# Performance work log

Measured on AMD Instinct MI355X. Metric: run time of the kernel, lower is better.

## Reference

```python
import jax, jax.numpy as jnp
import numpy as np
import math

B, L, IN_DIM = 2, 2048, 32
D_MODEL, NHEAD, D_FF, N_LAYERS, NUM_CLASSES = 256, 8, 1024, 2, 8
FACTOR = 5
D_K = D_MODEL // NHEAD
U = min(L, int(FACTOR * math.log(L)))  # ProbSparse top-k size = 38
LN_EPS = 1e-5


def setup_inputs() -> dict:
    key = jax.random.key(0)
    ks = jax.random.split(key, 16)
    s = 0.02
    d = {
        "x": jax.random.normal(ks[0], (B, L, IN_DIM), jnp.float32),
        "emb_w": jax.random.normal(ks[1], (IN_DIM, D_MODEL), jnp.float32) * s,
        "emb_b": jnp.zeros((D_MODEL,), jnp.float32),
        "wq": jax.random.normal(ks[2], (N_LAYERS, D_MODEL, D_MODEL), jnp.float32) * s,
        "bq": jnp.zeros((N_LAYERS, D_MODEL), jnp.float32),
        "wk": jax.random.normal(ks[3], (N_LAYERS, D_MODEL, D_MODEL), jnp.float32) * s,
        "bk": jnp.zeros((N_LAYERS, D_MODEL), jnp.float32),
        "wv": jax.random.normal(ks[4], (N_LAYERS, D_MODEL, D_MODEL), jnp.float32) * s,
        "bv": jnp.zeros((N_LAYERS, D_MODEL), jnp.float32),
        "wo": jax.random.normal(ks[5], (N_LAYERS, D_MODEL, D_MODEL), jnp.float32) * s,
        "bo": jnp.zeros((N_LAYERS, D_MODEL), jnp.float32),
        "ln1_g": jnp.ones((N_LAYERS, D_MODEL), jnp.float32),
        "ln1_b": jnp.zeros((N_LAYERS, D_MODEL), jnp.float32),
        "ln2_g": jnp.ones((N_LAYERS, D_MODEL), jnp.float32),
        "ln2_b": jnp.zeros((N_LAYERS, D_MODEL), jnp.float32),
        "ff1_w": jax.random.normal(ks[6], (N_LAYERS, D_MODEL, D_FF), jnp.float32) * s,
        "ff1_b": jnp.zeros((N_LAYERS, D_FF), jnp.float32),
        "ff2_w": jax.random.normal(ks[7], (N_LAYERS, D_FF, D_MODEL), jnp.float32) * s,
        "ff2_b": jnp.zeros((N_LAYERS, D_MODEL), jnp.float32),
        "dec_w": jax.random.normal(ks[8], (D_MODEL, NUM_CLASSES), jnp.float32) * s,
        "dec_b": jnp.zeros((NUM_CLASSES,), jnp.float32),
    }
    return d


def _pos_encoding(L, d):
    pos = jnp.arange(L, dtype=jnp.float32)[:, None]              # [L,1]
    div = jnp.exp(jnp.arange(0, d, 2, dtype=jnp.float32) * (-math.log(10000.0) / d))
    sin, cos = jnp.sin(pos * div), jnp.cos(pos * div)            # [L,d/2]
    return jnp.stack([sin, cos], axis=-1).reshape(L, d)          # interleave sin/cos


def _layernorm(h, g, b):
    m = jnp.mean(h, axis=-1, keepdims=True)
    v = jnp.mean((h - m) ** 2, axis=-1, keepdims=True)
    return (h - m) * jax.lax.rsqrt(v + LN_EPS) * g + b


def _prob_sparse_attn(h, wq, bq, wk, bk, wv, bv, wo, bo):
    Bb, Ll, _ = h.shape
    q = (h @ wq + bq).reshape(Bb, Ll, NHEAD, D_K).transpose(0, 2, 1, 3)  # [B,H,L,D]
    k = (h @ wk + bk).reshape(Bb, Ll, NHEAD, D_K).transpose(0, 2, 1, 3)
    v = (h @ wv + bv).reshape(Bb, Ll, NHEAD, D_K).transpose(0, 2, 1, 3)
    scores = jnp.einsum('bhld,bhmd->bhlm', q, k) / math.sqrt(D_K)        # [B,H,L,L]
    thr = jax.lax.top_k(scores, U)[0][..., -1:]                          # U-th largest per row
    scores = jnp.where(scores >= thr, scores, -jnp.inf)
    attn = jax.nn.softmax(scores, axis=-1)
    ctx = jnp.einsum('bhlm,bhmd->bhld', attn, v)
    ctx = ctx.transpose(0, 2, 1, 3).reshape(Bb, Ll, D_MODEL)
    return ctx @ wo + bo


def reference(x, emb_w, emb_b, wq, bq, wk, bk, wv, bv, wo, bo,
              ln1_g, ln1_b, ln2_g, ln2_b, ff1_w, ff1_b, ff2_w, ff2_b,
              dec_w, dec_b):
    h = (x @ emb_w + emb_b) * math.sqrt(D_MODEL)
    h = h + _pos_encoding(h.shape[1], D_MODEL)[None]
    for l in range(N_LAYERS):
        a = _prob_sparse_attn(h, wq[l], bq[l], wk[l], bk[l], wv[l], bv[l], wo[l], bo[l])
        h = _layernorm(h + a, ln1_g[l], ln1_b[l])
        ff = jax.nn.relu(h @ ff1_w[l] + ff1_b[l]) @ ff2_w[l] + ff2_b[l]
        h = _layernorm(h + ff, ln2_g[l], ln2_b[l])
    return h @ dec_w + dec_b
```

## Files before the change

kernel.cpp:

```cpp
#include <hip/hip_runtime.h>
#include <math.h>

#define D_MODEL 256
#define NHEAD   8
#define D_K     32
#define LSEQ    2048
#define BATCH   2
#define ROWS    (BATCH * LSEQ)
#define D_FF    1024
#define UTOP    38
#define CAP     128

__global__ __launch_bounds__(256) void k_embed(const float* __restrict__ x,
                                               const float* __restrict__ w,
                                               const float* __restrict__ b,
                                               float* __restrict__ h) {
    int row = blockIdx.x;
    int l   = row & (LSEQ - 1);
    int d   = threadIdx.x;
    __shared__ float xs[32];
    if (d < 32) xs[d] = x[row * 32 + d];
    __syncthreads();
    float acc = 0.f;
#pragma unroll
    for (int i = 0; i < 32; ++i) acc += xs[i] * w[i * D_MODEL + d];
    acc = (acc + b[d]) * 16.0f;
    int m = d >> 1;
    float div = expf(-(float)(2 * m) * (9.210340371976184f / 256.0f));
    float ang = (float)l * div;
    float pe = (d & 1) ? cosf(ang) : sinf(ang);
    h[row * D_MODEL + d] = acc + pe;
}

template <int MODE>
__device__ __forceinline__ void gemm_body(const float* __restrict__ A, int lda,
                                          const float* __restrict__ W, int N,
                                          const float* __restrict__ bias, bool doBias,
                                          float* __restrict__ C, int K,
                                          int m0, int n0) {
    __shared__ float As[16][68];
    __shared__ float Ws[16][68];
    const int t  = threadIdx.x;
    const int tx = t & 15, ty = t >> 4;
    float acc[4][4] = {};
    for (int k0 = 0; k0 < K; k0 += 16) {
        {
            int mr = t >> 2, kc = (t & 3) * 4;
            float4 av = *(const float4*)&A[(size_t)(m0 + mr) * lda + k0 + kc];
            As[kc + 0][mr] = av.x; As[kc + 1][mr] = av.y;
            As[kc + 2][mr] = av.z; As[kc + 3][mr] = av.w;
            int kr = t >> 4, nc = (t & 15) * 4;
            *(float4*)&Ws[kr][nc] = *(const float4*)&W[(size_t)(k0 + kr) * N + n0 + nc];
        }
        __syncthreads();
#pragma unroll
        for (int k = 0; k < 16; ++k) {
            float4 a4 = *(const float4*)&As[k][ty * 4];
            float4 w4 = *(const float4*)&Ws[k][tx * 4];
            float av[4] = {a4.x, a4.y, a4.z, a4.w};
            float wv[4] = {w4.x, w4.y, w4.z, w4.w};
#pragma unroll
            for (int i = 0; i < 4; ++i)
#pragma unroll
                for (int j = 0; j < 4; ++j) acc[i][j] += av[i] * wv[j];
        }
        __syncthreads();
    }
#pragma unroll
    for (int i = 0; i < 4; ++i) {
        int row = m0 + ty * 4 + i;
#pragma unroll
        for (int j = 0; j < 4; ++j) {
            int col = n0 + tx * 4 + j;
            float v = acc[i][j];
            if (doBias) v += bias[col];
            if (MODE == 1) v = fmaxf(v, 0.f);
            if (MODE == 2) {
                int bb = row >> 11, ll = row & (LSEQ - 1);
                int hh = col >> 5, dd = col & 31;
                C[(((size_t)(bb * NHEAD + hh) * LSEQ) + ll) * D_K + dd] = v;
            } else {
                C[(size_t)row * N + col] = v;
            }
        }
    }
}

__global__ __launch_bounds__(256) void k_qkv(const float* __restrict__ A,
                                             const float* __restrict__ wq,
                                             const float* __restrict__ wk,
                                             const float* __restrict__ wv,
                                             const float* __restrict__ bq,
                                             const float* __restrict__ bk,
                                             const float* __restrict__ bv,
                                             float* __restrict__ out) {
    int z = blockIdx.z;
    const float* W = z == 0 ? wq : (z == 1 ? wk : wv);
    const float* B = z == 0 ? bq : (z == 1 ? bk : bv);
    gemm_body<2>(A, 256, W, 256, B, true, out + (size_t)z * (1 << 20), 256,
                 blockIdx.x * 64, blockIdx.y * 64);
}

__global__ __launch_bounds__(256) void k_gemm_sk(const float* __restrict__ A, int lda,
                                                 const float* __restrict__ W,
                                                 const float* __restrict__ bias,
                                                 float* __restrict__ Cbase,
                                                 int N, int Ksub) {
    int z = blockIdx.z;
    gemm_body<0>(A + (size_t)z * Ksub, lda, W + (size_t)z * Ksub * N, N, bias, z == 0,
                 Cbase + (size_t)z * (1 << 20), Ksub, blockIdx.x * 64, blockIdx.y * 64);
}

__global__ __launch_bounds__(256) void k_ff1(const float* __restrict__ A,
                                             const float* __restrict__ W,
                                             const float* __restrict__ bias,
                                             float* __restrict__ C) {
    gemm_body<1>(A, 256, W, 1024, bias, true, C, 256, blockIdx.x * 64, blockIdx.y * 64);
}

__device__ __forceinline__ unsigned int sortkey(float f) {
    unsigned int u = __float_as_uint(f);
    return (u & 0x80000000u) ? ~u : (u | 0x80000000u);
}
__device__ __forceinline__ float key2f(unsigned int u) {
    unsigned int b = (u & 0x80000000u) ? (u ^ 0x80000000u) : ~u;
    return __uint_as_float(b);
}
__device__ __forceinline__ void gload_lds16(const float* src, float* ldsDst) {
    __builtin_amdgcn_global_load_lds(
        (const __attribute__((address_space(1))) unsigned int*)src,
        (__attribute__((address_space(3))) unsigned int*)ldsDst,
        16, 0, 0);
}

__global__ __launch_bounds__(256, 3) void k_attn(const float* __restrict__ Q,
                                                 const float* __restrict__ Kt,
                                                 const float* __restrict__ Vt,
                                                 float* __restrict__ ctxb) {
    __shared__ float          Kl[3][2048];
    __shared__ unsigned int   lvk[4][2][CAP];
    __shared__ unsigned short lix[4][2][CAP];
    __shared__ int            lcnt[4][2];

    const int tid   = threadIdx.x;
    const int lane  = tid & 63;
    const int wid   = tid >> 6;
    const int lbid  = (blockIdx.x & 7) * 512 + (blockIdx.x >> 3);
    const int bh    = lbid >> 8;
    const int chunk = lbid & 255;
    const int row0  = chunk * 8 + wid * 2;
    const int b     = bh >> 3, hh = bh & 7;
    const int h     = lane >> 5;
    const int p     = lane & 31;

    const float* Kb = Kt + (size_t)bh * LSEQ * D_K;
    const float* Vb = Vt + (size_t)bh * LSEQ * D_K;
    const float* qp = Q + ((size_t)bh * LSEQ + row0) * D_K;

    const float scale = 0.17677669529663687f;
    float q0[16], q1[16];
#pragma unroll
    for (int i = 0; i < 16; ++i) {
        q0[i] = qp[h * 16 + i] * scale;
        q1[i] = qp[32 + h * 16 + i] * scale;
    }

#define STAGE(T, SLOT)                                                          \
    {                                                                           \
        const int g0_ = wid * 2, g1_ = wid * 2 + 1;                             \
        gload_lds16(Kb + (size_t)(T) * 2048 + (2 * p + (g0_ >> 2)) * 32         \
                        + h * 16 + (g0_ & 3) * 4, &Kl[SLOT][g0_ * 256]);        \
        gload_lds16(Kb + (size_t)(T) * 2048 + (2 * p + (g1_ >> 2)) * 32         \
                        + h * 16 + (g1_ & 3) * 4, &Kl[SLOT][g1_ * 256]);        \
    }

    unsigned int k0[32], k1[32];
    unsigned int lm0 = 0u, lm1 = 0u;

    STAGE(0, 0)
    STAGE(1, 1)
    asm volatile("s_waitcnt vmcnt(2)" ::: "memory");
    __builtin_amdgcn_s_barrier();

#pragma unroll
    for (int t = 0; t < 32; ++t) {
        const int slot = t % 3;
        if (t < 30) STAGE(t + 2, (t + 2) % 3)
        float a0 = 0.f, a1 = 0.f, e0 = 0.f, e1 = 0.f;
#pragma unroll
        for (int c = 0; c < 4; ++c) {
            float4 kva = *(const float4*)&Kl[slot][c * 256 + lane * 4];
            float4 kvb = *(const float4*)&Kl[slot][(4 + c) * 256 + lane * 4];
            a0 += q0[c*4+0]*kva.x + q0[c*4+1]*kva.y + q0[c*4+2]*kva.z + q0[c*4+3]*kva.w;
            a1 += q1[c*4+0]*kva.x + q1[c*4+1]*kva.y + q1[c*4+2]*kva.z + q1[c*4+3]*kva.w;
            e0 += q0[c*4+0]*kvb.x + q0[c*4+1]*kvb.y + q0[c*4+2]*kvb.z + q0[c*4+3]*kvb.w;
            e1 += q1[c*4+0]*kvb.x + q1[c*4+1]*kvb.y + q1[c*4+2]*kvb.z + q1[c*4+3]*kvb.w;
        }
        float fA0 = a0 + __shfl_xor(a0, 32);
        float fB0 = e0 + __shfl_xor(e0, 32);
        float fA1 = a1 + __shfl_xor(a1, 32);
        float fB1 = e1 + __shfl_xor(e1, 32);
        k0[t] = sortkey(h ? fB0 : fA0);
        k1[t] = sortkey(h ? fB1 : fA1);
        if (k0[t] > lm0) lm0 = k0[t];
        if (k1[t] > lm1) lm1 = k1[t];
        if (t < 31) {
            if (t < 30) asm volatile("s_waitcnt vmcnt(2)" ::: "memory");
            else        asm volatile("s_waitcnt vmcnt(0)" ::: "memory");
            __builtin_amdgcn_s_barrier();
        }
    }

    unsigned int Tpiv[2];
    float        rmaxf[2];
#pragma unroll
    for (int r = 0; r < 2; ++r) {
        unsigned int v = r ? lm1 : lm0;
#pragma unroll
        for (int k = 2; k <= 64; k <<= 1) {
#pragma unroll
            for (int j = k >> 1; j >= 1; j >>= 1) {
                unsigned int pv = (unsigned int)__shfl_xor((int)v, j);
                bool lower = ((lane & j) == 0);
                bool up    = ((lane & k) == 0);
                unsigned int mn = v < pv ? v : pv;
                unsigned int mx = v < pv ? pv : v;
                v = (lower == up) ? mn : mx;
            }
        }
        Tpiv[r]  = (unsigned int)__shfl((int)v, 26);
        rmaxf[r] = key2f((unsigned int)__shfl((int)v, 63));
    }
    if (lane < 2) lcnt[wid][lane] = 0;

#pragma unroll
    for (int j = 0; j < 32; ++j) {
        if (k0[j] >= Tpiv[0]) {
            int s = atomicAdd(&lcnt[wid][0], 1);
            if (s < CAP) { lvk[wid][0][s] = k0[j]; lix[wid][0][s] = (unsigned short)(j * 64 + 2 * p + h); }
        }
        if (k1[j] >= Tpiv[1]) {
            int s = atomicAdd(&lcnt[wid][1], 1);
            if (s < CAP) { lvk[wid][1][s] = k1[j]; lix[wid][1][s] = (unsigned short)(j * 64 + 2 * p + h); }
        }
    }

#pragma unroll
    for (int r = 0; r < 2; ++r) {
        int cnt = lcnt[wid][r]; if (cnt > CAP) cnt = CAP;

        unsigned int v0 = (lane < cnt)      ? lvk[wid][r][lane]      : 0u;
        unsigned int v1 = (64 + lane < cnt) ? lvk[wid][r][64 + lane] : 0u;
#pragma unroll
        for (int k = 2; k <= 128; k <<= 1) {
#pragma unroll
            for (int j = k >> 1; j >= 1; j >>= 1) {
                if (j >= 64) {
                    bool up0 = ((lane & k) == 0);
                    unsigned int mn = v0 < v1 ? v0 : v1;
                    unsigned int mx = v0 < v1 ? v1 : v0;
                    v0 = up0 ? mn : mx;
                    v1 = up0 ? mx : mn;
                } else {
                    unsigned int p0 = (unsigned int)__shfl_xor((int)v0, j);
                    unsigned int p1 = (unsigned int)__shfl_xor((int)v1, j);
                    bool lower = ((lane & j) == 0);
                    bool up0 = (((lane) & k) == 0);
                    bool up1 = (((64 + lane) & k) == 0);
                    v0 = (lower == up0) ? (v0 < p0 ? v0 : p0) : (v0 < p0 ? p0 : v0);
                    v1 = (lower == up1) ? (v1 < p1 ? v1 : p1) : (v1 < p1 ? p1 : v1);
                }
            }
        }
        const unsigned int thrkey = (unsigned int)__shfl((int)v1, 26);

        float psum = 0.f;
        for (int i = lane; i < cnt; i += 64) {
            unsigned int key = lvk[wid][r][i];
            if (key >= thrkey) psum += expf(key2f(key) - rmaxf[r]);
        }
#pragma unroll
        for (int off = 32; off >= 1; off >>= 1) psum += __shfl_xor(psum, off);
        float inv = 1.0f / psum;

        float acc = 0.f;
        for (int i = h; i < cnt; i += 2) {
            unsigned int key = lvk[wid][r][i];
            float w = (key >= thrkey) ? expf(key2f(key) - rmaxf[r]) : 0.f;
            acc += w * Vb[(size_t)lix[wid][r][i] * D_K + p];
        }
        acc += __shfl_xor(acc, 32);
        if (lane < 32)
            ctxb[((size_t)(b * LSEQ) + row0 + r) * D_MODEL + hh * D_K + p] = acc * inv;
    }
}

__global__ __launch_bounds__(64) void k_addln2(float* __restrict__ h,
                                               const float* __restrict__ a1,
                                               const float* __restrict__ a2,
                                               const float* __restrict__ g,
                                               const float* __restrict__ bb) {
    int row = blockIdx.x, lane = threadIdx.x;
    float4 hv = *(const float4*)&h[(size_t)row * D_MODEL + lane * 4];
    float4 v1 = *(const float4*)&a1[(size_t)row * D_MODEL + lane * 4];
    float4 v2 = *(const float4*)&a2[(size_t)row * D_MODEL + lane * 4];
    float x0 = hv.x + v1.x + v2.x, x1 = hv.y + v1.y + v2.y;
    float x2 = hv.z + v1.z + v2.z, x3 = hv.w + v1.w + v2.w;
    float s = x0 + x1 + x2 + x3;
#pragma unroll
    for (int off = 32; off >= 1; off >>= 1) s += __shfl_xor(s, off);
    float mean = s * (1.0f / 256.0f);
    float d0 = x0 - mean, d1 = x1 - mean, d2 = x2 - mean, d3 = x3 - mean;
    float vs = d0 * d0 + d1 * d1 + d2 * d2 + d3 * d3;
#pragma unroll
    for (int off = 32; off >= 1; off >>= 1) vs += __shfl_xor(vs, off);
    float inv = rsqrtf(vs * (1.0f / 256.0f) + 1e-5f);
    float4 gv = *(const float4*)&g[lane * 4];
    float4 bv = *(const float4*)&bb[lane * 4];
    float4 o;
    o.x = d0 * inv * gv.x + bv.x;
    o.y = d1 * inv * gv.y + bv.y;
    o.z = d2 * inv * gv.z + bv.z;
    o.w = d3 * inv * gv.w + bv.w;
    *(float4*)&h[(size_t)row * D_MODEL + lane * 4] = o;
}

__global__ __launch_bounds__(64) void k_dec(const float* __restrict__ h,
                                            const float* __restrict__ w,
                                            const float* __restrict__ b,
                                            float* __restrict__ out) {
    int row = blockIdx.x, lane = threadIdx.x;
    int c = lane & 7, part = lane >> 3;
    float acc = 0.f;
    int d0 = part * 32;
#pragma unroll
    for (int dd = 0; dd < 32; ++dd) acc += h[(size_t)row * D_MODEL + d0 + dd] * w[(d0 + dd) * 8 + c];
    acc += __shfl_xor(acc, 8);
    acc += __shfl_xor(acc, 16);
    acc += __shfl_xor(acc, 32);
    if (lane < 8) out[(size_t)row * 8 + c] = acc + b[c];
}

extern "C" void kernel_launch(void* const* d_in, const int* in_sizes, int n_in,
                              void* d_out, int out_size, void* d_ws, size_t ws_size,
                              hipStream_t stream) {
    const float* x     = (const float*)d_in[0];
    const float* emb_w = (const float*)d_in[1];
    const float* emb_b = (const float*)d_in[2];
    const float* wq    = (const float*)d_in[3];
    const float* bq    = (const float*)d_in[4];
    const float* wk    = (const float*)d_in[5];
    const float* bk    = (const float*)d_in[6];
    const float* wv    = (const float*)d_in[7];
    const float* bv    = (const float*)d_in[8];
    const float* wo    = (const float*)d_in[9];
    const float* bo    = (const float*)d_in[10];
    const float* ln1_g = (const float*)d_in[11];
    const float* ln1_b = (const float*)d_in[12];
    const float* ln2_g = (const float*)d_in[13];
    const float* ln2_b = (const float*)d_in[14];
    const float* ff1_w = (const float*)d_in[15];
    const float* ff1_b = (const float*)d_in[16];
    const float* ff2_w = (const float*)d_in[17];
    const float* ff2_b = (const float*)d_in[18];
    const float* dec_w = (const float*)d_in[19];
    const float* dec_b = (const float*)d_in[20];

    float* ws   = (float*)d_ws;
    float* h    = ws;
    float* qb   = h    + (1 << 20);
    float* kb   = qb   + (1 << 20);
    float* vb   = kb   + (1 << 20);
    float* ctxb = vb   + (1 << 20);
    float* ffb  = ctxb + (1 << 20);

    k_embed<<<ROWS, 256, 0, stream>>>(x, emb_w, emb_b, h);

    for (int l = 0; l < 2; ++l) {
        const float* wql = wq + (size_t)l * 65536;  const float* bql = bq + l * 256;
        const float* wkl = wk + (size_t)l * 65536;  const float* bkl = bk + l * 256;
        const float* wvl = wv + (size_t)l * 65536;  const float* bvl = bv + l * 256;
        const float* wol = wo + (size_t)l * 65536;  const float* bol = bo + l * 256;

        dim3 gq(64, 4, 3);
        k_qkv<<<gq, 256, 0, stream>>>(h, wql, wkl, wvl, bql, bkl, bvl, qb);

        k_attn<<<NHEAD * BATCH * 256, 256, 0, stream>>>(qb, kb, vb, ctxb);

        dim3 gsk(64, 4, 2);
        k_gemm_sk<<<gsk, 256, 0, stream>>>(ctxb, 256, wol, bol, qb, 256, 128);
        k_addln2<<<ROWS, 64, 0, stream>>>(h, qb, kb, ln1_g + l * 256, ln1_b + l * 256);

        dim3 gf1(64, 16);
        k_ff1<<<gf1, 256, 0, stream>>>(h, ff1_w + (size_t)l * 262144, ff1_b + l * 1024, ffb);

        k_gemm_sk<<<gsk, 256, 0, stream>>>(ffb, 1024, ff2_w + (size_t)l * 262144,
                                           ff2_b + l * 256, qb, 256, 512);
        k_addln2<<<ROWS, 64, 0, stream>>>(h, qb, kb, ln2_g + l * 256, ln2_b + l * 256);
    }

    k_dec<<<ROWS, 64, 0, stream>>>(h, dec_w, dec_b, (float*)d_out);
}
```

Measured before the change: 831.0 us.

## Process four query rows per wave with per-wave double-buffered K staging

```diff
diff --git a/kernel.cpp b/kernel.cpp
--- a/kernel.cpp
+++ b/kernel.cpp
@@ -133,22 +133,22 @@
         16, 0, 0);
 }
 
-__global__ __launch_bounds__(256, 3) void k_attn(const float* __restrict__ Q,
+__global__ __launch_bounds__(256, 2) void k_attn(const float* __restrict__ Q,
                                                  const float* __restrict__ Kt,
                                                  const float* __restrict__ Vt,
                                                  float* __restrict__ ctxb) {
-    __shared__ float          Kl[3][2048];
-    __shared__ unsigned int   lvk[4][2][CAP];
-    __shared__ unsigned short lix[4][2][CAP];
-    __shared__ int            lcnt[4][2];
+    __shared__ float          Kl[4][2][2048];
+    __shared__ unsigned int   lvk[4][4][CAP];
+    __shared__ unsigned short lix[4][4][CAP];
+    __shared__ int            lcnt[4][4];
 
     const int tid   = threadIdx.x;
     const int lane  = tid & 63;
     const int wid   = tid >> 6;
-    const int lbid  = (blockIdx.x & 7) * 512 + (blockIdx.x >> 3);
-    const int bh    = lbid >> 8;
-    const int chunk = lbid & 255;
-    const int row0  = chunk * 8 + wid * 2;
+    const int lbid  = (blockIdx.x & 7) * 256 + (blockIdx.x >> 3);
+    const int bh    = lbid >> 7;
+    const int chunk = lbid & 127;
+    const int row0  = chunk * 16 + wid * 4;
     const int b     = bh >> 3, hh = bh & 7;
     const int h     = lane >> 5;
     const int p     = lane & 31;
@@ -158,64 +158,76 @@
     const float* qp = Q + ((size_t)bh * LSEQ + row0) * D_K;
 
     const float scale = 0.17677669529663687f;
-    float q0[16], q1[16];
+    float q0[16], q1[16], q2[16], q3[16];
 #pragma unroll
     for (int i = 0; i < 16; ++i) {
-        q0[i] = qp[h * 16 + i] * scale;
-        q1[i] = qp[32 + h * 16 + i] * scale;
+        q0[i] = qp[      h * 16 + i] * scale;
+        q1[i] = qp[32  + h * 16 + i] * scale;
+        q2[i] = qp[64  + h * 16 + i] * scale;
+        q3[i] = qp[96  + h * 16 + i] * scale;
     }
 
 #define STAGE(T, SLOT)                                                          \
     {                                                                           \
-        const int g0_ = wid * 2, g1_ = wid * 2 + 1;                             \
-        gload_lds16(Kb + (size_t)(T) * 2048 + (2 * p + (g0_ >> 2)) * 32         \
-                        + h * 16 + (g0_ & 3) * 4, &Kl[SLOT][g0_ * 256]);        \
-        gload_lds16(Kb + (size_t)(T) * 2048 + (2 * p + (g1_ >> 2)) * 32         \
-                        + h * 16 + (g1_ & 3) * 4, &Kl[SLOT][g1_ * 256]);        \
-    }
-
-    unsigned int k0[32], k1[32];
-    unsigned int lm0 = 0u, lm1 = 0u;
+        _Pragma("unroll")                                                       \
+        for (int u = 0; u < 8; ++u) {                                           \
+            gload_lds16(Kb + (size_t)(T) * 2048 + (2 * p + (u >> 2)) * 32       \
+                            + h * 16 + (u & 3) * 4, &Kl[wid][SLOT][u * 256]);   \
+        }                                                                       \
+    }
+
+    unsigned int k0[32], k1[32], k2[32], k3[32];
+    unsigned int lm0 = 0u, lm1 = 0u, lm2 = 0u, lm3 = 0u;
 
     STAGE(0, 0)
     STAGE(1, 1)
-    asm volatile("s_waitcnt vmcnt(2)" ::: "memory");
-    __builtin_amdgcn_s_barrier();
 
 #pragma unroll
     for (int t = 0; t < 32; ++t) {
-        const int slot = t % 3;
-        if (t < 30) STAGE(t + 2, (t + 2) % 3)
-        float a0 = 0.f, a1 = 0.f, e0 = 0.f, e1 = 0.f;
+        const int slot = t & 1;
+        if (t < 31) asm volatile("s_waitcnt vmcnt(8)" ::: "memory");
+        else        asm volatile("s_waitcnt vmcnt(0)" ::: "memory");
+        float a0 = 0.f, a1 = 0.f, a2 = 0.f, a3 = 0.f;
+        float e0 = 0.f, e1 = 0.f, e2 = 0.f, e3 = 0.f;
 #pragma unroll
         for (int c = 0; c < 4; ++c) {
-            float4 kva = *(const float4*)&Kl[slot][c * 256 + lane * 4];
-            float4 kvb = *(const float4*)&Kl[slot][(4 + c) * 256 + lane * 4];
+            float4 kva = *(const float4*)&Kl[wid][slot][c * 256 + lane * 4];
+            float4 kvb = *(const float4*)&Kl[wid][slot][(4 + c) * 256 + lane * 4];
             a0 += q0[c*4+0]*kva.x + q0[c*4+1]*kva.y + q0[c*4+2]*kva.z + q0[c*4+3]*kva.w;
             a1 += q1[c*4+0]*kva.x + q1[c*4+1]*kva.y + q1[c*4+2]*kva.z + q1[c*4+3]*kva.w;
+            a2 += q2[c*4+0]*kva.x + q2[c*4+1]*kva.y + q2[c*4+2]*kva.z + q2[c*4+3]*kva.w;
+            a3 += q3[c*4+0]*kva.x + q3[c*4+1]*kva.y + q3[c*4+2]*kva.z + q3[c*4+3]*kva.w;
             e0 += q0[c*4+0]*kvb.x + q0[c*4+1]*kvb.y + q0[c*4+2]*kvb.z + q0[c*4+3]*kvb.w;
             e1 += q1[c*4+0]*kvb.x + q1[c*4+1]*kvb.y + q1[c*4+2]*kvb.z + q1[c*4+3]*kvb.w;
-        }
-        float fA0 = a0 + __shfl_xor(a0, 32);
-        float fB0 = e0 + __shfl_xor(e0, 32);
-        float fA1 = a1 + __shfl_xor(a1, 32);
-        float fB1 = e1 + __shfl_xor(e1, 32);
-        k0[t] = sortkey(h ? fB0 : fA0);
-        k1[t] = sortkey(h ? fB1 : fA1);
-        if (k0[t] > lm0) lm0 = k0[t];
-        if (k1[t] > lm1) lm1 = k1[t];
-        if (t < 31) {
-            if (t < 30) asm volatile("s_waitcnt vmcnt(2)" ::: "memory");
-            else        asm volatile("s_waitcnt vmcnt(0)" ::: "memory");
-            __builtin_amdgcn_s_barrier();
-        }
-    }
-
-    unsigned int Tpiv[2];
-    float        rmaxf[2];
-#pragma unroll
-    for (int r = 0; r < 2; ++r) {
-        unsigned int v = r ? lm1 : lm0;
+            e2 += q2[c*4+0]*kvb.x + q2[c*4+1]*kvb.y + q2[c*4+2]*kvb.z + q2[c*4+3]*kvb.w;
+            e3 += q3[c*4+0]*kvb.x + q3[c*4+1]*kvb.y + q3[c*4+2]*kvb.z + q3[c*4+3]*kvb.w;
+        }
+        if (t < 30) STAGE(t + 2, slot)
+        {
+            float fa = a0 + __shfl_xor(a0, 32);
+            float fe = e0 + __shfl_xor(e0, 32);
+            k0[t] = sortkey(h ? fe : fa);
+            if (k0[t] > lm0) lm0 = k0[t];
+            fa = a1 + __shfl_xor(a1, 32);
+            fe = e1 + __shfl_xor(e1, 32);
+            k1[t] = sortkey(h ? fe : fa);
+            if (k1[t] > lm1) lm1 = k1[t];
+            fa = a2 + __shfl_xor(a2, 32);
+            fe = e2 + __shfl_xor(e2, 32);
+            k2[t] = sortkey(h ? fe : fa);
+            if (k2[t] > lm2) lm2 = k2[t];
+            fa = a3 + __shfl_xor(a3, 32);
+            fe = e3 + __shfl_xor(e3, 32);
+            k3[t] = sortkey(h ? fe : fa);
+            if (k3[t] > lm3) lm3 = k3[t];
+        }
+    }
+
+    unsigned int Tpiv[4];
+    float        rmaxf[4];
+#pragma unroll
+    for (int r = 0; r < 4; ++r) {
+        unsigned int v = (r == 0) ? lm0 : (r == 1) ? lm1 : (r == 2) ? lm2 : lm3;
 #pragma unroll
         for (int k = 2; k <= 64; k <<= 1) {
 #pragma unroll
@@ -231,22 +243,26 @@
         Tpiv[r]  = (unsigned int)__shfl((int)v, 26);
         rmaxf[r] = key2f((unsigned int)__shfl((int)v, 63));
     }
-    if (lane < 2) lcnt[wid][lane] = 0;
-
-#pragma unroll
-    for (int j = 0; j < 32; ++j) {
-        if (k0[j] >= Tpiv[0]) {
-            int s = atomicAdd(&lcnt[wid][0], 1);
-            if (s < CAP) { lvk[wid][0][s] = k0[j]; lix[wid][0][s] = (unsigned short)(j * 64 + 2 * p + h); }
-        }
-        if (k1[j] >= Tpiv[1]) {
-            int s = atomicAdd(&lcnt[wid][1], 1);
-            if (s < CAP) { lvk[wid][1][s] = k1[j]; lix[wid][1][s] = (unsigned short)(j * 64 + 2 * p + h); }
-        }
-    }
-
-#pragma unroll
-    for (int r = 0; r < 2; ++r) {
+    if (lane < 4) lcnt[wid][lane] = 0;
+
+#define PUSHROW(KARR, R)                                                        \
+    _Pragma("unroll")                                                           \
+    for (int j = 0; j < 32; ++j) {                                              \
+        if (KARR[j] >= Tpiv[R]) {                                               \
+            int s = atomicAdd(&lcnt[wid][R], 1);                                \
+            if (s < CAP) {                                                      \
+                lvk[wid][R][s] = KARR[j];                                       \
+                lix[wid][R][s] = (unsigned short)(j * 64 + 2 * p + h);          \
+            }                                                                   \
+        }                                                                       \
+    }
+    PUSHROW(k0, 0)
+    PUSHROW(k1, 1)
+    PUSHROW(k2, 2)
+    PUSHROW(k3, 3)
+
+#pragma unroll
+    for (int r = 0; r < 4; ++r) {
         int cnt = lcnt[wid][r]; if (cnt > CAP) cnt = CAP;
 
         unsigned int v0 = (lane < cnt)      ? lvk[wid][r][lane]      : 0u;
@@ -385,7 +401,7 @@
         dim3 gq(64, 4, 3);
         k_qkv<<<gq, 256, 0, stream>>>(h, wql, wkl, wvl, bql, bkl, bvl, qb);
 
-        k_attn<<<NHEAD * BATCH * 256, 256, 0, stream>>>(qb, kb, vb, ctxb);
+        k_attn<<<NHEAD * BATCH * 128, 256, 0, stream>>>(qb, kb, vb, ctxb);
 
         dim3 gsk(64, 4, 2);
         k_gemm_sk<<<gsk, 256, 0, stream>>>(ctxb, 256, wol, bol, qb, 256, 128);
```

Measured after the change: 1.103 ms. +32.8%, slower.

## Process one query row per wave in attention kernel with full-dim dot per lane

Applied to the files above, without the earlier changes.

```diff
diff --git a/kernel.cpp b/kernel.cpp
--- a/kernel.cpp
+++ b/kernel.cpp
@@ -133,49 +133,44 @@
         16, 0, 0);
 }
 
-__global__ __launch_bounds__(256, 3) void k_attn(const float* __restrict__ Q,
+__global__ __launch_bounds__(256, 5) void k_attn(const float* __restrict__ Q,
                                                  const float* __restrict__ Kt,
                                                  const float* __restrict__ Vt,
                                                  float* __restrict__ ctxb) {
     __shared__ float          Kl[3][2048];
-    __shared__ unsigned int   lvk[4][2][CAP];
-    __shared__ unsigned short lix[4][2][CAP];
-    __shared__ int            lcnt[4][2];
+    __shared__ unsigned int   lvk[4][CAP];
+    __shared__ unsigned short lix[4][CAP];
+    __shared__ int            lcnt[4];
 
     const int tid   = threadIdx.x;
     const int lane  = tid & 63;
     const int wid   = tid >> 6;
-    const int lbid  = (blockIdx.x & 7) * 512 + (blockIdx.x >> 3);
-    const int bh    = lbid >> 8;
-    const int chunk = lbid & 255;
-    const int row0  = chunk * 8 + wid * 2;
+    const int lbid  = (blockIdx.x & 7) * 1024 + (blockIdx.x >> 3);
+    const int bh    = lbid >> 9;
+    const int chunk = lbid & 511;
+    const int row   = chunk * 4 + wid;
     const int b     = bh >> 3, hh = bh & 7;
-    const int h     = lane >> 5;
-    const int p     = lane & 31;
 
     const float* Kb = Kt + (size_t)bh * LSEQ * D_K;
     const float* Vb = Vt + (size_t)bh * LSEQ * D_K;
-    const float* qp = Q + ((size_t)bh * LSEQ + row0) * D_K;
+    const float* qp = Q + ((size_t)bh * LSEQ + row) * D_K;
 
     const float scale = 0.17677669529663687f;
-    float q0[16], q1[16];
-#pragma unroll
-    for (int i = 0; i < 16; ++i) {
-        q0[i] = qp[h * 16 + i] * scale;
-        q1[i] = qp[32 + h * 16 + i] * scale;
-    }
+    float q[32];
+#pragma unroll
+    for (int i = 0; i < 32; ++i) q[i] = qp[i] * scale;
 
 #define STAGE(T, SLOT)                                                          \
     {                                                                           \
         const int g0_ = wid * 2, g1_ = wid * 2 + 1;                             \
-        gload_lds16(Kb + (size_t)(T) * 2048 + (2 * p + (g0_ >> 2)) * 32         \
-                        + h * 16 + (g0_ & 3) * 4, &Kl[SLOT][g0_ * 256]);        \
-        gload_lds16(Kb + (size_t)(T) * 2048 + (2 * p + (g1_ >> 2)) * 32         \
-                        + h * 16 + (g1_ & 3) * 4, &Kl[SLOT][g1_ * 256]);        \
-    }
-
-    unsigned int k0[32], k1[32];
-    unsigned int lm0 = 0u, lm1 = 0u;
+        gload_lds16(Kb + (size_t)(T) * 2048 + lane * 32 + g0_ * 4,              \
+                    &Kl[SLOT][g0_ * 256]);                                      \
+        gload_lds16(Kb + (size_t)(T) * 2048 + lane * 32 + g1_ * 4,              \
+                    &Kl[SLOT][g1_ * 256]);                                      \
+    }
+
+    unsigned int kk[32];
+    unsigned int lm = 0u;
 
     STAGE(0, 0)
     STAGE(1, 1)
@@ -186,24 +181,14 @@
     for (int t = 0; t < 32; ++t) {
         const int slot = t % 3;
         if (t < 30) STAGE(t + 2, (t + 2) % 3)
-        float a0 = 0.f, a1 = 0.f, e0 = 0.f, e1 = 0.f;
-#pragma unroll
-        for (int c = 0; c < 4; ++c) {
-            float4 kva = *(const float4*)&Kl[slot][c * 256 + lane * 4];
-            float4 kvb = *(const float4*)&Kl[slot][(4 + c) * 256 + lane * 4];
-            a0 += q0[c*4+0]*kva.x + q0[c*4+1]*kva.y + q0[c*4+2]*kva.z + q0[c*4+3]*kva.w;
-            a1 += q1[c*4+0]*kva.x + q1[c*4+1]*kva.y + q1[c*4+2]*kva.z + q1[c*4+3]*kva.w;
-            e0 += q0[c*4+0]*kvb.x + q0[c*4+1]*kvb.y + q0[c*4+2]*kvb.z + q0[c*4+3]*kvb.w;
-            e1 += q1[c*4+0]*kvb.x + q1[c*4+1]*kvb.y + q1[c*4+2]*kvb.z + q1[c*4+3]*kvb.w;
-        }
-        float fA0 = a0 + __shfl_xor(a0, 32);
-        float fB0 = e0 + __shfl_xor(e0, 32);
-        float fA1 = a1 + __shfl_xor(a1, 32);
-        float fB1 = e1 + __shfl_xor(e1, 32);
-        k0[t] = sortkey(h ? fB0 : fA0);
-        k1[t] = sortkey(h ? fB1 : fA1);
-        if (k0[t] > lm0) lm0 = k0[t];
-        if (k1[t] > lm1) lm1 = k1[t];
+        float a = 0.f;
+#pragma unroll
+        for (int u = 0; u < 8; ++u) {
+            float4 kv = *(const float4*)&Kl[slot][u * 256 + lane * 4];
+            a += q[u*4+0]*kv.x + q[u*4+1]*kv.y + q[u*4+2]*kv.z + q[u*4+3]*kv.w;
+        }
+        kk[t] = sortkey(a);
+        if (kk[t] > lm) lm = kk[t];
         if (t < 31) {
             if (t < 30) asm volatile("s_waitcnt vmcnt(2)" ::: "memory");
             else        asm volatile("s_waitcnt vmcnt(0)" ::: "memory");
@@ -211,11 +196,10 @@
         }
     }
 
-    unsigned int Tpiv[2];
-    float        rmaxf[2];
-#pragma unroll
-    for (int r = 0; r < 2; ++r) {
-        unsigned int v = r ? lm1 : lm0;
+    unsigned int Tpiv;
+    float        rmaxf;
+    {
+        unsigned int v = lm;
 #pragma unroll
         for (int k = 2; k <= 64; k <<= 1) {
 #pragma unroll
@@ -228,71 +212,69 @@
                 v = (lower == up) ? mn : mx;
             }
         }
-        Tpiv[r]  = (unsigned int)__shfl((int)v, 26);
-        rmaxf[r] = key2f((unsigned int)__shfl((int)v, 63));
-    }
-    if (lane < 2) lcnt[wid][lane] = 0;
+        Tpiv  = (unsigned int)__shfl((int)v, 26);
+        rmaxf = key2f((unsigned int)__shfl((int)v, 63));
+    }
+    if (lane == 0) lcnt[wid] = 0;
 
 #pragma unroll
     for (int j = 0; j < 32; ++j) {
-        if (k0[j] >= Tpiv[0]) {
-            int s = atomicAdd(&lcnt[wid][0], 1);
-            if (s < CAP) { lvk[wid][0][s] = k0[j]; lix[wid][0][s] = (unsigned short)(j * 64 + 2 * p + h); }
-        }
-        if (k1[j] >= Tpiv[1]) {
-            int s = atomicAdd(&lcnt[wid][1], 1);
-            if (s < CAP) { lvk[wid][1][s] = k1[j]; lix[wid][1][s] = (unsigned short)(j * 64 + 2 * p + h); }
-        }
-    }
-
-#pragma unroll
-    for (int r = 0; r < 2; ++r) {
-        int cnt = lcnt[wid][r]; if (cnt > CAP) cnt = CAP;
-
-        unsigned int v0 = (lane < cnt)      ? lvk[wid][r][lane]      : 0u;
-        unsigned int v1 = (64 + lane < cnt) ? lvk[wid][r][64 + lane] : 0u;
-#pragma unroll
-        for (int k = 2; k <= 128; k <<= 1) {
-#pragma unroll
-            for (int j = k >> 1; j >= 1; j >>= 1) {
-                if (j >= 64) {
-                    bool up0 = ((lane & k) == 0);
-                    unsigned int mn = v0 < v1 ? v0 : v1;
-                    unsigned int mx = v0 < v1 ? v1 : v0;
-                    v0 = up0 ? mn : mx;
-                    v1 = up0 ? mx : mn;
-                } else {
-                    unsigned int p0 = (unsigned int)__shfl_xor((int)v0, j);
-                    unsigned int p1 = (unsigned int)__shfl_xor((int)v1, j);
-                    bool lower = ((lane & j) == 0);
-                    bool up0 = (((lane) & k) == 0);
-                    bool up1 = (((64 + lane) & k) == 0);
-                    v0 = (lower == up0) ? (v0 < p0 ? v0 : p0) : (v0 < p0 ? p0 : v0);
-                    v1 = (lower == up1) ? (v1 < p1 ? v1 : p1) : (v1 < p1 ? p1 : v1);
-                }
+        if (kk[j] >= Tpiv) {
+            int s = atomicAdd(&lcnt[wid], 1);
+            if (s < CAP) {
+                lvk[wid][s] = kk[j];
+                lix[wid][s] = (unsigned short)(j * 64 + lane);
             }
         }
-        const unsigned int thrkey = (unsigned int)__shfl((int)v1, 26);
-
-        float psum = 0.f;
-        for (int i = lane; i < cnt; i += 64) {
-            unsigned int key = lvk[wid][r][i];
-            if (key >= thrkey) psum += expf(key2f(key) - rmaxf[r]);
-        }
-#pragma unroll
-        for (int off = 32; off >= 1; off >>= 1) psum += __shfl_xor(psum, off);
-        float inv = 1.0f / psum;
-
-        float acc = 0.f;
-        for (int i = h; i < cnt; i += 2) {
-            unsigned int key = lvk[wid][r][i];
-            float w = (key >= thrkey) ? expf(key2f(key) - rmaxf[r]) : 0.f;
-            acc += w * Vb[(size_t)lix[wid][r][i] * D_K + p];
-        }
-        acc += __shfl_xor(acc, 32);
-        if (lane < 32)
-            ctxb[((size_t)(b * LSEQ) + row0 + r) * D_MODEL + hh * D_K + p] = acc * inv;
-    }
+    }
+
+    int cnt = lcnt[wid]; if (cnt > CAP) cnt = CAP;
+
+    unsigned int v0 = (lane < cnt)      ? lvk[wid][lane]      : 0u;
+    unsigned int v1 = (64 + lane < cnt) ? lvk[wid][64 + lane] : 0u;
+#pragma unroll
+    for (int k = 2; k <= 128; k <<= 1) {
+#pragma unroll
+        for (int j = k >> 1; j >= 1; j >>= 1) {
+            if (j >= 64) {
+                bool up0 = ((lane & k) == 0);
+                unsigned int mn = v0 < v1 ? v0 : v1;
+                unsigned int mx = v0 < v1 ? v1 : v0;
+                v0 = up0 ? mn : mx;
+                v1 = up0 ? mx : mn;
+            } else {
+                unsigned int p0 = (unsigned int)__shfl_xor((int)v0, j);
+                unsigned int p1 = (unsigned int)__shfl_xor((int)v1, j);
+                bool lower = ((lane & j) == 0);
+                bool up0 = (((lane) & k) == 0);
+                bool up1 = (((64 + lane) & k) == 0);
+                v0 = (lower == up0) ? (v0 < p0 ? v0 : p0) : (v0 < p0 ? p0 : v0);
+                v1 = (lower == up1) ? (v1 < p1 ? v1 : p1) : (v1 < p1 ? p1 : v1);
+            }
+        }
+    }
+    const unsigned int thrkey = (unsigned int)__shfl((int)v1, 26);
+
+    float psum = 0.f;
+    for (int i = lane; i < cnt; i += 64) {
+        unsigned int key = lvk[wid][i];
+        if (key >= thrkey) psum += expf(key2f(key) - rmaxf);
+    }
+#pragma unroll
+    for (int off = 32; off >= 1; off >>= 1) psum += __shfl_xor(psum, off);
+    float inv = 1.0f / psum;
+
+    const int h = lane >> 5;
+    const int p = lane & 31;
+    float acc = 0.f;
+    for (int i = h; i < cnt; i += 2) {
+        unsigned int key = lvk[wid][i];
+        float w = (key >= thrkey) ? expf(key2f(key) - rmaxf) : 0.f;
+        acc += w * Vb[(size_t)lix[wid][i] * D_K + p];
+    }
+    acc += __shfl_xor(acc, 32);
+    if (lane < 32)
+        ctxb[((size_t)(b * LSEQ) + row) * D_MODEL + hh * D_K + p] = acc * inv;
 }
 
 __global__ __launch_bounds__(64) void k_addln2(float* __restrict__ h,
@@ -385,7 +367,7 @@
         dim3 gq(64, 4, 3);
         k_qkv<<<gq, 256, 0, stream>>>(h, wql, wkl, wvl, bql, bkl, bvl, qb);
 
-        k_attn<<<NHEAD * BATCH * 256, 256, 0, stream>>>(qb, kb, vb, ctxb);
+        k_attn<<<NHEAD * BATCH * 512, 256, 0, stream>>>(qb, kb, vb, ctxb);
 
         dim3 gsk(64, 4, 2);
         k_gemm_sk<<<gsk, 256, 0, stream>>>(ctxb, 256, wol, bol, qb, 256, 128);
```

Result: slower. 1.702 ms (+104.8%).
